# Performance work log

Hardware: AMD Instinct MI355X
Metric: run time of the kernel (lower is better)

Reference implementation:

```python
import jax, jax.numpy as jnp
import numpy as np

B, M, K, C = 256, 512, 6, 32  # graphs, nodes/graph, knn k, channels
IN_DIM, OUT_DIM = 4, 6


def setup_inputs() -> dict:
    key = jax.random.key(0)
    ks = jax.random.split(key, 20)
    N = B * M
    x = jax.random.normal(ks[0], (N, 1), dtype=jnp.float32)
    pos = jax.random.uniform(ks[1], (N, 3), dtype=jnp.float32)
    batch = jnp.repeat(jnp.arange(B, dtype=jnp.int64), M)

    def lin(k, out_d, in_d):
        bound = 1.0 / np.sqrt(in_d)
        kw, kb = jax.random.split(k)
        W = jax.random.uniform(kw, (out_d, in_d), minval=-bound, maxval=bound, dtype=jnp.float32)
        b = jax.random.uniform(kb, (out_d,), minval=-bound, maxval=bound, dtype=jnp.float32)
        return W, b

    W1a, b1a = lin(ks[2], C, IN_DIM)
    W2a, b2a = lin(ks[3], C, C)
    W1b, b1b = lin(ks[4], C, C)
    W2b, b2b = lin(ks[5], C, C)
    W1c, b1c = lin(ks[6], C, C)
    W2c, b2c = lin(ks[7], C, C)
    Wr, br = lin(ks[8], OUT_DIM, C)
    return dict(x=x, pos=pos, batch=batch,
                W1a=W1a, b1a=b1a, W2a=W2a, b2a=b2a,
                W1b=W1b, b1b=b1b, W2b=W2b, b2b=b2b,
                W1c=W1c, b1c=b1c, W2c=W2c, b2c=b2c,
                Wr=Wr, br=br)


def knn_indices(pos3):
    # pos3: [B, M, 3] -> [B, M, K] indices of K nearest neighbors (self included, loop=True)
    sq = jnp.sum(pos3 * pos3, axis=-1)                      # [B, M]
    d2 = sq[:, :, None] + sq[:, None, :] - 2.0 * jnp.einsum('bmd,bnd->bmn', pos3, pos3)
    _, idx = jax.lax.top_k(-d2, K)                          # [B, M, K]
    return idx


def gcn_layer(h, idx, W1, b1, W2, b2):
    # h: [B, M, Cin]; gather h_j per edge, 2-layer MLP per edge, max-aggregate over neighbors
    Cin = h.shape[-1]
    nb = jnp.take_along_axis(h, idx.reshape(B, M * K, 1), axis=1).reshape(B, M, K, Cin)
    msg = jax.nn.relu(jnp.einsum('bmkc,oc->bmko', nb, W1) + b1)
    msg = jnp.einsum('bmkc,oc->bmko', msg, W2) + b2
    return jnp.max(msg, axis=2)                             # max aggregation -> [B, M, C]


def reference(x, pos, batch,
              W1a, b1a, W2a, b2a,
              W1b, b1b, W2b, b2b,
              W1c, b1c, W2c, b2c,
              Wr, br):
    pos3 = pos.reshape(B, M, 3)
    idx = knn_indices(pos3)
    h = jnp.concatenate([x, pos], axis=-1).reshape(B, M, IN_DIM)
    h = jax.nn.relu(gcn_layer(h, idx, W1a, b1a, W2a, b2a))
    h = jax.nn.relu(gcn_layer(h, idx, W1b, b1b, W2b, b2b))
    h = jax.nn.relu(gcn_layer(h, idx, W1c, b1c, W2c, b2c))
    g = jnp.max(h, axis=1)                                  # global_max_pool -> [B, C]
    return g @ Wr.T + br                                    # [B, 6]
```

## Files before the change

kernel.cpp:

```cpp
#include <hip/hip_runtime.h>
#include <cstddef>

#define NB 256
#define M 512
#define KNN 6
#define C 32

__global__ __launch_bounds__(1024, 1) void megafused_kernel(
    const float* __restrict__ x, const float* __restrict__ pos,
    const float* __restrict__ W1a, const float* __restrict__ b1a,
    const float* __restrict__ W2a, const float* __restrict__ b2a,
    const float* __restrict__ W1b, const float* __restrict__ b1b,
    const float* __restrict__ W2b, const float* __restrict__ b2b,
    const float* __restrict__ W1c, const float* __restrict__ b1c,
    const float* __restrict__ W2c, const float* __restrict__ b2c,
    const float* __restrict__ Wr,  const float* __restrict__ br,
    float* __restrict__ out)
{
    __shared__ __align__(16) float Ts[M * C];
    const int g  = blockIdx.x;
    const int t  = threadIdx.x;
    const int n  = t & (M - 1);
    const int hv = t >> 9;
    const int c0 = __builtin_amdgcn_readfirstlane(hv << 4);

    float4* sp          = (float4*)Ts;
    float*  cd          = Ts + 2048;
    unsigned short* ci  = (unsigned short*)(Ts + 2048 + 7168);

    const float* p = pos + (size_t)g * M * 3;
    if (t < M) {
        float xx = p[3*t], yy = p[3*t+1], zz = p[3*t+2];
        sp[t] = make_float4(xx, yy, zz, fmaf(xx, xx, fmaf(yy, yy, zz * zz)));
    }
    __syncthreads();

    const float4 pm = sp[n];

    float d[KNN]; int id[KNN];
#pragma unroll
    for (int k = 0; k < KNN; k++) { d[k] = INFINITY; id[k] = -1; }

    const int col0 = hv << 8;
#pragma unroll 4
    for (int jj = 0; jj < 256; jj++) {
        const int col = col0 + jj;
        const float4 pn = sp[col];
        float dot  = fmaf(pm.x, pn.x, fmaf(pm.y, pn.y, pm.z * pn.z));
        float dist = fmaf(-2.f, dot, pm.w + pn.w);
#pragma unroll
        for (int k = KNN - 1; k > 0; k--) {
            bool ck  = dist < d[k];
            bool ck1 = dist < d[k - 1];
            d[k]  = ck1 ? d[k - 1]  : (ck ? dist : d[k]);
            id[k] = ck1 ? id[k - 1] : (ck ? col  : id[k]);
        }
        bool c0b = dist < d[0];
        d[0]  = c0b ? dist : d[0];
        id[0] = c0b ? col  : id[0];
    }
#pragma unroll
    for (int k = 0; k < KNN; k++) {
        cd[t * 7 + k] = d[k];
        ci[t * 7 + k] = (unsigned short)id[k];
    }
    __syncthreads();

    int j[KNN];
    {
        float md[KNN]; int mi[KNN];
#pragma unroll
        for (int k = 0; k < KNN; k++) { md[k] = cd[n*7 + k]; mi[k] = ci[n*7 + k]; }
        const int L1 = (n + M) * 7;
#pragma unroll
        for (int k = 0; k < KNN; k++) {
            float dist = cd[L1 + k];
            int   nn   = ci[L1 + k];
#pragma unroll
            for (int q = KNN - 1; q > 0; q--) {
                bool cq  = dist < md[q];
                bool cq1 = dist < md[q - 1];
                md[q] = cq1 ? md[q - 1] : (cq ? dist : md[q]);
                mi[q] = cq1 ? mi[q - 1] : (cq ? nn   : mi[q]);
            }
            bool cb = dist < md[0];
            md[0] = cb ? dist : md[0];
            mi[0] = cb ? nn   : mi[0];
        }
#pragma unroll
        for (int k = 0; k < KNN; k++) j[k] = mi[k];
    }
    __syncthreads();

    const int np = n & 7;

    {
        const float h0 = x[(size_t)g * M + n];
        const float h1 = pm.x, h2 = pm.y, h3 = pm.z;
        float m1[C];
#pragma unroll
        for (int o = 0; o < C; o++) {
            float a = b1a[o];
            a = fmaf(W1a[o*4+0], h0, a);
            a = fmaf(W1a[o*4+1], h1, a);
            a = fmaf(W1a[o*4+2], h2, a);
            a = fmaf(W1a[o*4+3], h3, a);
            m1[o] = fmaxf(a, 0.f);
        }
#pragma unroll
        for (int q2 = 0; q2 < 4; q2++) {
            float4 v; float* vp = &v.x;
#pragma unroll
            for (int u = 0; u < 4; u++) {
                const int o = c0 + q2*4 + u;
                float a = b2a[o];
#pragma unroll
                for (int i = 0; i < C; i++) a = fmaf(W2a[o*C + i], m1[i], a);
                vp[u] = a;
            }
            const int q = 4*hv + q2;
            *(float4*)&Ts[n*C + ((q ^ np) << 2)] = v;
        }
    }
    __syncthreads();

#pragma unroll 1
    for (int layer = 0; layer < 2; layer++) {
        const float* W1 = layer ? W1c : W1b;
        const float* b1 = layer ? b1c : b1b;
        const float* W2 = layer ? W2c : W2b;
        const float* b2 = layer ? b2c : b2b;

        float hm[16];
#pragma unroll
        for (int u = 0; u < 16; u++) hm[u] = -INFINITY;
#pragma unroll
        for (int k = 0; k < KNN; k++) {
            const int jl = j[k], jp = jl & 7;
#pragma unroll
            for (int q2 = 0; q2 < 4; q2++) {
                const int q = 4*hv + q2;
                const float4 v = *(const float4*)&Ts[jl*C + ((q ^ jp) << 2)];
                hm[4*q2+0] = fmaxf(hm[4*q2+0], v.x);
                hm[4*q2+1] = fmaxf(hm[4*q2+1], v.y);
                hm[4*q2+2] = fmaxf(hm[4*q2+2], v.z);
                hm[4*q2+3] = fmaxf(hm[4*q2+3], v.w);
            }
        }
#pragma unroll
        for (int u = 0; u < 16; u++) hm[u] = fmaxf(hm[u], 0.f);
        __syncthreads();
#pragma unroll
        for (int q2 = 0; q2 < 4; q2++) {
            const int q = 4*hv + q2;
            *(float4*)&Ts[n*C + ((q ^ np) << 2)] =
                make_float4(hm[4*q2], hm[4*q2+1], hm[4*q2+2], hm[4*q2+3]);
        }
        __syncthreads();
        float hf[C];
#pragma unroll
        for (int q = 0; q < 8; q++) {
            const float4 v = *(const float4*)&Ts[n*C + ((q ^ np) << 2)];
            hf[4*q+0] = v.x; hf[4*q+1] = v.y; hf[4*q+2] = v.z; hf[4*q+3] = v.w;
        }
        __syncthreads();
        float m1[C];
#pragma unroll
        for (int o = 0; o < C; o++) {
            float a = b1[o];
#pragma unroll
            for (int i = 0; i < C; i++) a = fmaf(W1[o*C + i], hf[i], a);
            m1[o] = fmaxf(a, 0.f);
        }
#pragma unroll
        for (int q2 = 0; q2 < 4; q2++) {
            float4 v; float* vp = &v.x;
#pragma unroll
            for (int u = 0; u < 4; u++) {
                const int o = c0 + q2*4 + u;
                float a = b2[o];
#pragma unroll
                for (int i = 0; i < C; i++) a = fmaf(W2[o*C + i], m1[i], a);
                vp[u] = a;
            }
            const int q = 4*hv + q2;
            *(float4*)&Ts[n*C + ((q ^ np) << 2)] = v;
        }
        __syncthreads();
    }

    {
        float hm[16];
#pragma unroll
        for (int u = 0; u < 16; u++) hm[u] = -INFINITY;
#pragma unroll
        for (int k = 0; k < KNN; k++) {
            const int jl = j[k], jp = jl & 7;
#pragma unroll
            for (int q2 = 0; q2 < 4; q2++) {
                const int q = 4*hv + q2;
                const float4 v = *(const float4*)&Ts[jl*C + ((q ^ jp) << 2)];
                hm[4*q2+0] = fmaxf(hm[4*q2+0], v.x);
                hm[4*q2+1] = fmaxf(hm[4*q2+1], v.y);
                hm[4*q2+2] = fmaxf(hm[4*q2+2], v.z);
                hm[4*q2+3] = fmaxf(hm[4*q2+3], v.w);
            }
        }
        __syncthreads();
#pragma unroll
        for (int q2 = 0; q2 < 4; q2++) {
            const int q = 4*hv + q2;
            *(float4*)&Ts[n*C + ((q ^ np) << 2)] =
                make_float4(fmaxf(hm[4*q2+0], 0.f), fmaxf(hm[4*q2+1], 0.f),
                            fmaxf(hm[4*q2+2], 0.f), fmaxf(hm[4*q2+3], 0.f));
        }
        __syncthreads();
    }

    const int tp = t & 7;
    for (int s = 256; s >= 32; s >>= 1) {
        if (t < s) {
#pragma unroll
            for (int q = 0; q < 8; q++) {
                const int ph = (q ^ tp) << 2;
                float4 a = *(const float4*)&Ts[t*C + ph];
                float4 b = *(const float4*)&Ts[(t + s)*C + ph];
                a.x = fmaxf(a.x, b.x); a.y = fmaxf(a.y, b.y);
                a.z = fmaxf(a.z, b.z); a.w = fmaxf(a.w, b.w);
                *(float4*)&Ts[t*C + ph] = a;
            }
        }
        __syncthreads();
    }

    if (t < C) {
        float m = -INFINITY;
#pragma unroll
        for (int r = 0; r < 32; r++)
            m = fmaxf(m, Ts[r*C + ((((t >> 2) ^ (r & 7)) << 2) | (t & 3))]);
        Ts[t] = m;
    }
    __syncthreads();

    if (t < 6) {
        float a = br[t];
#pragma unroll
        for (int i = 0; i < C; i++) a = fmaf(Wr[t*C + i], Ts[i], a);
        out[g * 6 + t] = a;
    }
}

extern "C" void kernel_launch(void* const* d_in, const int* in_sizes, int n_in,
                              void* d_out, int out_size, void* d_ws, size_t ws_size,
                              hipStream_t stream) {
    const float* x   = (const float*)d_in[0];
    const float* pos = (const float*)d_in[1];
    const float* W1a = (const float*)d_in[3];
    const float* b1a = (const float*)d_in[4];
    const float* W2a = (const float*)d_in[5];
    const float* b2a = (const float*)d_in[6];
    const float* W1b = (const float*)d_in[7];
    const float* b1b = (const float*)d_in[8];
    const float* W2b = (const float*)d_in[9];
    const float* b2b = (const float*)d_in[10];
    const float* W1c = (const float*)d_in[11];
    const float* b1c = (const float*)d_in[12];
    const float* W2c = (const float*)d_in[13];
    const float* b2c = (const float*)d_in[14];
    const float* Wr  = (const float*)d_in[15];
    const float* br  = (const float*)d_in[16];

    float* out = (float*)d_out;

    megafused_kernel<<<NB, 1024, 0, stream>>>(x, pos,
                                              W1a, b1a, W2a, b2a,
                                              W1b, b1b, W2b, b2b,
                                              W1c, b1c, W2c, b2c,
                                              Wr, br, out);
}
```

Measured before the change: 202.1 us.

## Use med3 insertion for kNN, split first MLP across half-blocks, fold ReLU into max init

The kNN top-6 insertion now computes the sorted distances with fmed3/fmin instead of paired compare-select chains, which shortens the per-candidate dependency chain. In the inner GCN layers the first MLP layer is split so each half of the block computes 16 of the 32 outputs. The halves then exchange results through shared memory with an extra barrier, which removes the duplicated W1 matvec. The separate ReLU pass is dropped by starting the max-aggregation at 0, at the cost of more syncs and LDS traffic per layer.

```diff
diff --git a/kernel.cpp b/kernel.cpp
--- a/kernel.cpp
+++ b/kernel.cpp
@@ -37,9 +37,9 @@
 
     const float4 pm = sp[n];
 
-    float d[KNN]; int id[KNN];
-#pragma unroll
-    for (int k = 0; k < KNN; k++) { d[k] = INFINITY; id[k] = -1; }
+    float d0 = INFINITY, d1 = INFINITY, d2 = INFINITY,
+          d3 = INFINITY, d4 = INFINITY, d5 = INFINITY;
+    int   i0 = -1, i1 = -1, i2 = -1, i3 = -1, i4 = -1, i5 = -1;
 
     const int col0 = hv << 8;
 #pragma unroll 4
@@ -48,21 +48,28 @@
         const float4 pn = sp[col];
         float dot  = fmaf(pm.x, pn.x, fmaf(pm.y, pn.y, pm.z * pn.z));
         float dist = fmaf(-2.f, dot, pm.w + pn.w);
-#pragma unroll
-        for (int k = KNN - 1; k > 0; k--) {
-            bool ck  = dist < d[k];
-            bool ck1 = dist < d[k - 1];
-            d[k]  = ck1 ? d[k - 1]  : (ck ? dist : d[k]);
-            id[k] = ck1 ? id[k - 1] : (ck ? col  : id[k]);
-        }
-        bool c0b = dist < d[0];
-        d[0]  = c0b ? dist : d[0];
-        id[0] = c0b ? col  : id[0];
-    }
-#pragma unroll
-    for (int k = 0; k < KNN; k++) {
-        cd[t * 7 + k] = d[k];
-        ci[t * 7 + k] = (unsigned short)id[k];
+        bool c5 = dist < d5, c4 = dist < d4, c3 = dist < d3,
+             c2 = dist < d2, c1 = dist < d1, cz = dist < d0;
+        i5 = c4 ? i4 : (c5 ? col : i5);
+        i4 = c3 ? i3 : (c4 ? col : i4);
+        i3 = c2 ? i2 : (c3 ? col : i3);
+        i2 = c1 ? i1 : (c2 ? col : i2);
+        i1 = cz ? i0 : (c1 ? col : i1);
+        i0 = cz ? col : i0;
+        d5 = __builtin_amdgcn_fmed3f(dist, d4, d5);
+        d4 = __builtin_amdgcn_fmed3f(dist, d3, d4);
+        d3 = __builtin_amdgcn_fmed3f(dist, d2, d3);
+        d2 = __builtin_amdgcn_fmed3f(dist, d1, d2);
+        d1 = __builtin_amdgcn_fmed3f(dist, d0, d1);
+        d0 = fminf(dist, d0);
+    }
+    {
+        float* cdp = cd + t * 7;
+        cdp[0]=d0; cdp[1]=d1; cdp[2]=d2; cdp[3]=d3; cdp[4]=d4; cdp[5]=d5;
+        unsigned short* cip = ci + t * 7;
+        cip[0]=(unsigned short)i0; cip[1]=(unsigned short)i1;
+        cip[2]=(unsigned short)i2; cip[3]=(unsigned short)i3;
+        cip[4]=(unsigned short)i4; cip[5]=(unsigned short)i5;
     }
     __syncthreads();
 
@@ -76,16 +83,20 @@
         for (int k = 0; k < KNN; k++) {
             float dist = cd[L1 + k];
             int   nn   = ci[L1 + k];
-#pragma unroll
-            for (int q = KNN - 1; q > 0; q--) {
-                bool cq  = dist < md[q];
-                bool cq1 = dist < md[q - 1];
-                md[q] = cq1 ? md[q - 1] : (cq ? dist : md[q]);
-                mi[q] = cq1 ? mi[q - 1] : (cq ? nn   : mi[q]);
-            }
-            bool cb = dist < md[0];
-            md[0] = cb ? dist : md[0];
-            mi[0] = cb ? nn   : mi[0];
+            bool c5 = dist < md[5], c4 = dist < md[4], c3 = dist < md[3],
+                 c2 = dist < md[2], c1 = dist < md[1], cz = dist < md[0];
+            mi[5] = c4 ? mi[4] : (c5 ? nn : mi[5]);
+            mi[4] = c3 ? mi[3] : (c4 ? nn : mi[4]);
+            mi[3] = c2 ? mi[2] : (c3 ? nn : mi[3]);
+            mi[2] = c1 ? mi[1] : (c2 ? nn : mi[2]);
+            mi[1] = cz ? mi[0] : (c1 ? nn : mi[1]);
+            mi[0] = cz ? nn : mi[0];
+            md[5] = __builtin_amdgcn_fmed3f(dist, md[4], md[5]);
+            md[4] = __builtin_amdgcn_fmed3f(dist, md[3], md[4]);
+            md[3] = __builtin_amdgcn_fmed3f(dist, md[2], md[3]);
+            md[2] = __builtin_amdgcn_fmed3f(dist, md[1], md[2]);
+            md[1] = __builtin_amdgcn_fmed3f(dist, md[0], md[1]);
+            md[0] = fminf(dist, md[0]);
         }
 #pragma unroll
         for (int k = 0; k < KNN; k++) j[k] = mi[k];
@@ -133,7 +144,7 @@
 
         float hm[16];
 #pragma unroll
-        for (int u = 0; u < 16; u++) hm[u] = -INFINITY;
+        for (int u = 0; u < 16; u++) hm[u] = 0.f;
 #pragma unroll
         for (int k = 0; k < KNN; k++) {
             const int jl = j[k], jp = jl & 7;
@@ -147,8 +158,6 @@
                 hm[4*q2+3] = fmaxf(hm[4*q2+3], v.w);
             }
         }
-#pragma unroll
-        for (int u = 0; u < 16; u++) hm[u] = fmaxf(hm[u], 0.f);
         __syncthreads();
 #pragma unroll
         for (int q2 = 0; q2 < 4; q2++) {
@@ -164,14 +173,29 @@
             hf[4*q+0] = v.x; hf[4*q+1] = v.y; hf[4*q+2] = v.z; hf[4*q+3] = v.w;
         }
         __syncthreads();
+        float m1h[16];
+#pragma unroll
+        for (int o2 = 0; o2 < 16; o2++) {
+            const int o = c0 + o2;
+            float a = b1[o];
+#pragma unroll
+            for (int i = 0; i < C; i++) a = fmaf(W1[o*C + i], hf[i], a);
+            m1h[o2] = fmaxf(a, 0.f);
+        }
+#pragma unroll
+        for (int q2 = 0; q2 < 4; q2++) {
+            const int q = 4*hv + q2;
+            *(float4*)&Ts[n*C + ((q ^ np) << 2)] =
+                make_float4(m1h[4*q2], m1h[4*q2+1], m1h[4*q2+2], m1h[4*q2+3]);
+        }
+        __syncthreads();
         float m1[C];
 #pragma unroll
-        for (int o = 0; o < C; o++) {
-            float a = b1[o];
-#pragma unroll
-            for (int i = 0; i < C; i++) a = fmaf(W1[o*C + i], hf[i], a);
-            m1[o] = fmaxf(a, 0.f);
-        }
+        for (int q = 0; q < 8; q++) {
+            const float4 v = *(const float4*)&Ts[n*C + ((q ^ np) << 2)];
+            m1[4*q+0] = v.x; m1[4*q+1] = v.y; m1[4*q+2] = v.z; m1[4*q+3] = v.w;
+        }
+        __syncthreads();
 #pragma unroll
         for (int q2 = 0; q2 < 4; q2++) {
             float4 v; float* vp = &v.x;
@@ -192,7 +216,7 @@
     {
         float hm[16];
 #pragma unroll
-        for (int u = 0; u < 16; u++) hm[u] = -INFINITY;
+        for (int u = 0; u < 16; u++) hm[u] = 0.f;
 #pragma unroll
         for (int k = 0; k < KNN; k++) {
             const int jl = j[k], jp = jl & 7;
@@ -211,8 +235,7 @@
         for (int q2 = 0; q2 < 4; q2++) {
             const int q = 4*hv + q2;
             *(float4*)&Ts[n*C + ((q ^ np) << 2)] =
-                make_float4(fmaxf(hm[4*q2+0], 0.f), fmaxf(hm[4*q2+1], 0.f),
-                            fmaxf(hm[4*q2+2], 0.f), fmaxf(hm[4*q2+3], 0.f));
+                make_float4(hm[4*q2], hm[4*q2+1], hm[4*q2+2], hm[4*q2+3]);
         }
         __syncthreads();
     }
```

Result: faster. 180.2 us (-10.8%).
